# Kernel optimization log

Hardware: AMD Instinct MI355X
Metric: run time of the kernel (lower is better)

## Reference

```python
import jax, jax.numpy as jnp
import numpy as np

GN_GROUPS = 32
GN_EPS = 1e-5


def conv3x3(x, w, b=None):
    # x: [B,C,H,W], w: [O,I,3,3]
    y = jax.lax.conv_general_dilated(x, w, (1, 1), 'SAME',
                                     dimension_numbers=('NCHW', 'OIHW', 'NCHW'))
    if b is not None:
        y = y + b[None, :, None, None]
    return y


def group_norm(x, gamma, beta):
    B, C, H, W = x.shape
    xg = x.reshape(B, GN_GROUPS, C // GN_GROUPS, H, W)
    mu = xg.mean(axis=(2, 3, 4), keepdims=True)
    var = ((xg - mu) ** 2).mean(axis=(2, 3, 4), keepdims=True)
    xn = ((xg - mu) * jax.lax.rsqrt(var + GN_EPS)).reshape(B, C, H, W)
    return xn * gamma[None, :, None, None] + beta[None, :, None, None]


def tower(x, ws, gammas, betas):
    # ws: [n_conv, C, C, 3, 3]; conv(bias=False) -> GroupNorm -> ReLU, n_conv times
    for i in range(ws.shape[0]):
        x = jax.nn.relu(group_norm(conv3x3(x, ws[i]), gammas[i], betas[i]))
    return x


def setup_inputs() -> dict:
    key = jax.random.key(0)
    ks = jax.random.split(key, 20)
    C, n_conv, n_fg = 256, 4, 20  # n_class - 1 = 20
    prior = 0.01
    B = 2
    sizes = [(100, 100), (50, 50), (25, 25), (13, 13), (7, 7)]
    inp = {}
    for i, (h, w) in enumerate(sizes):
        inp[f'feat{i}'] = jax.random.normal(ks[i], (B, C, h, w), dtype=jnp.float32)
    std = 0.01  # init_conv_std
    inp['cls_tw_w'] = std * jax.random.normal(ks[5], (n_conv, C, C, 3, 3), dtype=jnp.float32)
    inp['cls_tw_g'] = jnp.ones((n_conv, C), dtype=jnp.float32)
    inp['cls_tw_b'] = jnp.zeros((n_conv, C), dtype=jnp.float32)
    inp['box_tw_w'] = std * jax.random.normal(ks[6], (n_conv, C, C, 3, 3), dtype=jnp.float32)
    inp['box_tw_g'] = jnp.ones((n_conv, C), dtype=jnp.float32)
    inp['box_tw_b'] = jnp.zeros((n_conv, C), dtype=jnp.float32)
    inp['cls_pred_w'] = std * jax.random.normal(ks[7], (n_fg, C, 3, 3), dtype=jnp.float32)
    prior_bias = -np.log((1.0 - prior) / prior)
    inp['cls_pred_b'] = jnp.full((n_fg,), prior_bias, dtype=jnp.float32)
    inp['box_pred_w'] = std * jax.random.normal(ks[8], (4, C, 3, 3), dtype=jnp.float32)
    inp['box_pred_b'] = jnp.zeros((4,), dtype=jnp.float32)
    inp['ctr_pred_w'] = std * jax.random.normal(ks[9], (1, C, 3, 3), dtype=jnp.float32)
    inp['ctr_pred_b'] = jnp.zeros((1,), dtype=jnp.float32)
    inp['scales'] = jnp.ones((5,), dtype=jnp.float32)
    return inp


def reference(feat0, feat1, feat2, feat3, feat4,
              cls_tw_w, cls_tw_g, cls_tw_b,
              box_tw_w, box_tw_g, box_tw_b,
              cls_pred_w, cls_pred_b,
              box_pred_w, box_pred_b,
              ctr_pred_w, ctr_pred_b,
              scales):
    feats = [feat0, feat1, feat2, feat3, feat4]
    logits, bboxes, centers = [], [], []
    for i, feat in enumerate(feats):
        c = tower(feat, cls_tw_w, cls_tw_g, cls_tw_b)
        logits.append(conv3x3(c, cls_pred_w, cls_pred_b))
        centers.append(conv3x3(c, ctr_pred_w, ctr_pred_b))
        b = tower(feat, box_tw_w, box_tw_g, box_tw_b)
        bboxes.append(jnp.exp(conv3x3(b, box_pred_w, box_pred_b) * scales[i]))
    return tuple(logits + bboxes + centers)
```

## Files before the change

kernel.cpp:

```cpp
#include <hip/hip_runtime.h>
#include <hip/hip_bf16.h>
#include <cstdint>

typedef unsigned short u16;
typedef __attribute__((ext_vector_type(8))) short short8;
typedef __attribute__((ext_vector_type(4))) float floatx4;
typedef __attribute__((ext_vector_type(4))) int intx4;

#define PA_TOTAL 13696
#define CCH 256
#define KTOT 2304

struct Tables {
  int H[5], W[5], P[5], base[5], tile0[5];
  int lb[5], bb[5], cb[5];
};
struct FeatPtrs { const float* f[5]; };
struct ConvArgs {
  const u16* X[2];
  const u16* Wt[2];
  const u16* zbuf;
  u16* outB[2];
  float* stats;
  float* dout;
  const float* biasCls; const float* biasCtr; const float* biasBox; const float* scales;
};

__device__ __forceinline__ u16 f2bf(float f) {
  union { float f; unsigned u; } v; v.f = f;
  unsigned r = v.u + 0x7fffu + ((v.u >> 16) & 1u);
  return (u16)(r >> 16);
}
__device__ __forceinline__ float bf2f(u16 h) {
  union { unsigned u; float f; } v; v.u = ((unsigned)h) << 16;
  return v.f;
}

__global__ void reorder_rows(const float* __restrict__ src, u16* __restrict__ out) {
  __shared__ float row[KTOT];
  const int r = blockIdx.x;
  const float* s = src + (size_t)r * KTOT;
  u16* o = out + (size_t)r * KTOT;
#pragma unroll
  for (int j = 0; j < 9; ++j) row[threadIdx.x + j * 256] = s[threadIdx.x + j * 256];
  __syncthreads();
#pragma unroll
  for (int j = 0; j < 9; ++j) {
    int k = threadIdx.x + j * 256;
    o[k] = f2bf(row[(k & 255) * 9 + (k >> 8)]);
  }
}

__global__ void reorder_pred_cls(const float* __restrict__ cls_w, const float* __restrict__ ctr_w,
                                 u16* __restrict__ out) {
  __shared__ float row[KTOT];
  const int r = blockIdx.x;
  const float* s = (r < 20) ? (cls_w + (size_t)r * KTOT) : ctr_w;
  u16* o = out + (size_t)r * KTOT;
#pragma unroll
  for (int j = 0; j < 9; ++j) row[threadIdx.x + j * 256] = s[threadIdx.x + j * 256];
  __syncthreads();
#pragma unroll
  for (int j = 0; j < 9; ++j) {
    int k = threadIdx.x + j * 256;
    o[k] = f2bf(row[(k & 255) * 9 + (k >> 8)]);
  }
}

__global__ void convert_inputs(FeatPtrs fp, u16* __restrict__ out, Tables tb) {
  __shared__ float tile[32][33];
  const int pt = blockIdx.x, c32 = blockIdx.y, b = blockIdx.z;
  const int p0 = pt * 32;
  int lvl = 0;
#pragma unroll
  for (int i = 1; i < 5; ++i) if (p0 >= tb.base[i]) lvl = i;
  const int P = tb.P[lvl];
  const int pl0 = p0 - tb.base[lvl];
  const int r = threadIdx.x >> 5, col = threadIdx.x & 31;
  const float* src = fp.f[lvl] + ((size_t)b * CCH + c32 * 32) * P;
#pragma unroll
  for (int i = 0; i < 4; ++i) {
    int crow = r + i * 8;
    int pl = pl0 + col;
    tile[crow][col] = (pl < P) ? src[(size_t)crow * P + pl] : 0.f;
  }
  __syncthreads();
#pragma unroll
  for (int i = 0; i < 4; ++i) {
    int px = r + i * 8;
    out[((size_t)b * PA_TOTAL + p0 + px) * CCH + c32 * 32 + col] = f2bf(tile[col][px]);
  }
}

template <int MODE>
__global__ __launch_bounds__(256) void conv_mfma(ConvArgs a, Tables tb) {
  constexpr int NI = (MODE == 0) ? 4 : 1;
  const int L = blockIdx.x + (MODE == 0 ? 107 : 108) * (blockIdx.y + 2 * blockIdx.z);
  const int xcd = L & 7, slot = L >> 3;
  int tower, mt, b, t;
  if (MODE == 0) {
    tower = xcd >> 2; mt = (xcd >> 1) & 1; b = xcd & 1; t = slot;
  } else {
    tower = xcd >> 2; mt = 0; b = (xcd >> 1) & 1; t = slot * 2 + (xcd & 1);
    if (t >= 107) return;
  }
  int lvl = 0;
#pragma unroll
  for (int i = 1; i < 5; ++i) if (t >= tb.tile0[i]) lvl = i;
  const int H = tb.H[lvl], W = tb.W[lvl], P = tb.P[lvl], base = tb.base[lvl];
  const int n0 = (t - tb.tile0[lvl]) * 128;

  const int tid = threadIdx.x;
  const int lane = tid & 63, wv = tid >> 6;
  const int wm = wv >> 1, wn = wv & 1;

  __shared__ u16 ldsX[128 * 64];
  __shared__ u16 ldsW[(MODE == 0 ? 128 : 32) * 64];

  const u16* X = a.X[tower];
  const u16* Wt = a.Wt[tower];

  const int qsw = (((lane & 7) ^ (lane >> 3))) * 8;
  int prow[4];
  unsigned mask9[4];
  int xdst[4];
#pragma unroll
  for (int t4 = 0; t4 < 4; ++t4) {
    int row = (t4 * 4 + wv) * 8 + (lane >> 3);
    prow[t4] = n0 + row;
    int rr = prow[t4] / W, cc = prow[t4] - rr * W;
    unsigned m = 0;
#pragma unroll
    for (int tap = 0; tap < 9; ++tap) {
      const int dh = tap / 3 - 1, dw = tap % 3 - 1;
      bool v = ((unsigned)(rr + dh) < (unsigned)H) & ((unsigned)(cc + dw) < (unsigned)W);
      m |= ((unsigned)v) << tap;
    }
    mask9[t4] = m;
    xdst[t4] = (t4 * 4 + wv) * 1024 + lane * 16;
  }
  const u16* wsrc[NI];
  int wdst[NI];
#pragma unroll
  for (int e = 0; e < NI; ++e) {
    int wrow = (MODE == 0) ? ((e * 4 + wv) * 8 + (lane >> 3)) : (wv * 8 + (lane >> 3));
    wsrc[e] = Wt + (size_t)(mt * 128 + wrow) * KTOT + qsw;
    wdst[e] = (MODE == 0) ? xdst[e] : (wv * 1024 + lane * 16);
  }
  const u16* Xbp = X + ((size_t)b * PA_TOTAL + base) * CCH;

  const int arow = lane & 15, rsw = lane & 7, kq0 = lane >> 4;
  int aoff[2][NI], boff[2][4];
#pragma unroll
  for (int h = 0; h < 2; ++h) {
    int csw = (((h * 4 + kq0) ^ rsw)) * 8;
#pragma unroll
    for (int i = 0; i < NI; ++i) {
      int rowb = (MODE == 0) ? (wm * 64 + i * 16) : (wm * 16);
      aoff[h][i] = (rowb + arow) * 64 + csw;
    }
#pragma unroll
    for (int i = 0; i < 4; ++i) boff[h][i] = (wn * 64 + i * 16 + arow) * 64 + csw;
  }

  floatx4 acc[NI][4];
#pragma unroll
  for (int i = 0; i < NI; ++i)
#pragma unroll
    for (int j = 0; j < 4; ++j) acc[i][j] = (floatx4)0.f;

  const intx4 zreg = {0, 0, 0, 0};
  intx4 xr[4], wr[NI];
  {
    const int dpos0 = -W - 1;
#pragma unroll
    for (int t4 = 0; t4 < 4; ++t4)
      xr[t4] = (mask9[t4] & 1)
          ? *(const intx4*)(Xbp + (size_t)(prow[t4] + dpos0) * CCH + qsw) : zreg;
#pragma unroll
    for (int e = 0; e < NI; ++e) wr[e] = *(const intx4*)(wsrc[e]);
  }

#pragma unroll 1
  for (int icb = 0; icb < 4; ++icb) {
#pragma unroll
    for (int tap = 0; tap < 9; ++tap) {
      __syncthreads();
#pragma unroll
      for (int t4 = 0; t4 < 4; ++t4) *(intx4*)((char*)ldsX + xdst[t4]) = xr[t4];
#pragma unroll
      for (int e = 0; e < NI; ++e) *(intx4*)((char*)ldsW + wdst[e]) = wr[e];
      if (!(icb == 3 && tap == 8)) {
        const int ntap = (tap == 8) ? 0 : tap + 1;
        const int nicb = (tap == 8) ? icb + 1 : icb;
        const int ndh = ntap / 3;
        const int ndpos = (ndh - 1) * W + (ntap - 3 * ndh - 1);
        const int nko = ntap * 256 + nicb * 64;
#pragma unroll
        for (int t4 = 0; t4 < 4; ++t4)
          xr[t4] = ((mask9[t4] >> ntap) & 1)
              ? *(const intx4*)(Xbp + (size_t)(prow[t4] + ndpos) * CCH + qsw + nicb * 64) : zreg;
#pragma unroll
        for (int e = 0; e < NI; ++e) wr[e] = *(const intx4*)(wsrc[e] + nko);
      }
      asm volatile("s_waitcnt lgkmcnt(0)\n\ts_barrier" ::: "memory");
#pragma unroll
      for (int h = 0; h < 2; ++h) {
        short8 af[NI], bv[4];
#pragma unroll
        for (int i = 0; i < NI; ++i) af[i] = *(const short8*)(ldsW + aoff[h][i]);
#pragma unroll
        for (int j = 0; j < 4; ++j) bv[j] = *(const short8*)(ldsX + boff[h][j]);
#pragma unroll
        for (int i = 0; i < NI; ++i)
#pragma unroll
          for (int j = 0; j < 4; ++j)
            acc[i][j] = __builtin_amdgcn_mfma_f32_16x16x32_bf16(af[i], bv[j], acc[i][j], 0, 0, 0);
      }
    }
  }

  const int quad = lane >> 4, col = lane & 15;
  if (MODE == 0) {
    u16* convB = a.outB[tower];
    float s[4] = {0.f, 0.f, 0.f, 0.f}, ss[4] = {0.f, 0.f, 0.f, 0.f};
#pragma unroll
    for (int j = 0; j < 4; ++j) {
      int pl = n0 + wn * 64 + j * 16 + col;
      bool valid = pl < P;
      u16* dst = convB + ((size_t)b * PA_TOTAL + base + pl) * CCH + mt * 128 + wm * 64 + quad * 4;
#pragma unroll
      for (int i = 0; i < 4; ++i) {
        ushort4 hv;
#pragma unroll
        for (int r = 0; r < 4; ++r) {
          u16 hh = f2bf(acc[i][j][r]);
          ((u16*)&hv)[r] = hh;
          float vr = bf2f(hh);
          if (valid) { s[i] += vr; ss[i] += vr * vr; }
        }
        if (valid) *(ushort4*)(dst + i * 16) = hv;
      }
    }
#pragma unroll
    for (int i = 0; i < 4; ++i) {
#pragma unroll
      for (int off = 16; off >= 1; off >>= 1) {
        s[i] += __shfl_down(s[i], off, 64);
        ss[i] += __shfl_down(ss[i], off, 64);
      }
    }
    if ((lane & 31) == 0) {
      int half = lane >> 5;
#pragma unroll
      for (int i = 0; i < 4; ++i) {
        float* st = a.stats + tower * 640 +
                    ((size_t)((b * 5 + lvl) * 32 + mt * 16 + wm * 8 + i * 2 + half)) * 2;
        atomicAdd(st, s[i]);
        atomicAdd(st + 1, ss[i]);
      }
    }
  } else {
    float* dout = a.dout;
    if (tower == 0) {
#pragma unroll
      for (int j = 0; j < 4; ++j) {
        int pl = n0 + wn * 64 + j * 16 + col;
        if (pl >= P) continue;
        int ocb = wm * 16 + quad * 4;
#pragma unroll
        for (int r = 0; r < 4; ++r) {
          int oc = ocb + r;
          float v = acc[0][j][r];
          if (oc < 20)       dout[tb.lb[lvl] + ((size_t)b * 20 + oc) * P + pl] = v + a.biasCls[oc];
          else if (oc == 20) dout[tb.cb[lvl] + (size_t)b * P + pl] = v + a.biasCtr[0];
        }
      }
    } else {
      float sc = a.scales[lvl];
#pragma unroll
      for (int j = 0; j < 4; ++j) {
        int pl = n0 + wn * 64 + j * 16 + col;
        if (pl >= P) continue;
        int ocb = wm * 16 + quad * 4;
#pragma unroll
        for (int r = 0; r < 4; ++r) {
          int oc = ocb + r;
          if (oc < 4)
            dout[tb.bb[lvl] + ((size_t)b * 4 + oc) * P + pl] = expf((acc[0][j][r] + a.biasBox[oc]) * sc);
        }
      }
    }
  }
}

__global__ void gn_norm(const u16* __restrict__ c0, const u16* __restrict__ c1,
                        const float* __restrict__ stats,
                        const float* __restrict__ g0, const float* __restrict__ b0,
                        const float* __restrict__ g1, const float* __restrict__ b1,
                        u16* __restrict__ a0, u16* __restrict__ a1, Tables tb) {
  const int tower = blockIdx.y;
  const u16* convB = tower ? c1 : c0;
  const float* gamma = tower ? g1 : g0;
  const float* beta = tower ? b1 : b0;
  u16* act = tower ? a1 : a0;
  int idx = blockIdx.x * 256 + threadIdx.x;
  int c8 = idx & 31;
  int rest = idx >> 5;
  int p = rest % PA_TOTAL;
  int b = rest / PA_TOTAL;
  int lvl = 0;
#pragma unroll
  for (int i = 1; i < 5; ++i) if (p >= tb.base[i]) lvl = i;
  if (p - tb.base[lvl] >= tb.P[lvl]) return;
  const float* st = stats + tower * 640 + ((size_t)((b * 5 + lvl) * 32 + c8)) * 2;
  float cnt = 8.f * (float)tb.P[lvl];
  float mean = st[0] / cnt;
  float var = st[1] / cnt - mean * mean;
  float inv = rsqrtf(var + 1e-5f);
  const short8 x = *(const short8*)(convB + ((size_t)b * PA_TOTAL + p) * CCH + c8 * 8);
  short8 o;
#pragma unroll
  for (int j = 0; j < 8; ++j) {
    float v = bf2f((u16)x[j]);
    float y = (v - mean) * inv * gamma[c8 * 8 + j] + beta[c8 * 8 + j];
    y = fmaxf(y, 0.f);
    o[j] = (short)f2bf(y);
  }
  *(short8*)(act + ((size_t)b * PA_TOTAL + p) * CCH + c8 * 8) = o;
}

extern "C" void kernel_launch(void* const* d_in, const int* in_sizes, int n_in,
                              void* d_out, int out_size, void* d_ws, size_t ws_size,
                              hipStream_t stream) {
  const float* feat[5];
  for (int i = 0; i < 5; ++i) feat[i] = (const float*)d_in[i];
  const float* cls_tw_w  = (const float*)d_in[5];
  const float* cls_tw_g  = (const float*)d_in[6];
  const float* cls_tw_b  = (const float*)d_in[7];
  const float* box_tw_w  = (const float*)d_in[8];
  const float* box_tw_g  = (const float*)d_in[9];
  const float* box_tw_b  = (const float*)d_in[10];
  const float* cls_pred_w = (const float*)d_in[11];
  const float* cls_pred_b = (const float*)d_in[12];
  const float* box_pred_w = (const float*)d_in[13];
  const float* box_pred_b = (const float*)d_in[14];
  const float* ctr_pred_w = (const float*)d_in[15];
  const float* ctr_pred_b = (const float*)d_in[16];
  const float* scales     = (const float*)d_in[17];
  float* out = (float*)d_out;

  char* ws = (char*)d_ws;
  u16*   zbuf   = (u16*)(ws);
  float* stats  = (float*)(ws + 512);
  u16*   WrCls  = (u16*)(ws + 8192);
  u16*   WrBox  = (u16*)(ws + 8192 + 4718592);
  u16*   WrPCls = (u16*)(ws + 8192 + 2 * 4718592);
  u16*   WrPBox = (u16*)(ws + 8192 + 2 * 4718592 + 589824);
  u16*   bufIn   = (u16*)(ws + 10625024);
  u16*   bufAct0 = (u16*)(ws + 10625024 + 1 * (size_t)14024704);
  u16*   bufAct1 = (u16*)(ws + 10625024 + 2 * (size_t)14024704);
  u16*   bufCv0  = (u16*)(ws + 10625024 + 3 * (size_t)14024704);
  u16*   bufCv1  = (u16*)(ws + 10625024 + 4 * (size_t)14024704);

  Tables tb = { {100,50,25,13,7}, {100,50,25,13,7}, {10000,2500,625,169,49},
                {0,10112,12672,13312,13568}, {0,79,99,104,106},
                {0,400000,500000,525000,531760},
                {533720,613720,633720,638720,640072},
                {640464,660464,665464,666714,667052} };

  hipMemsetAsync(zbuf, 0, 512, stream);
  hipMemsetAsync(WrPCls, 0, 589824, stream);
  hipMemsetAsync(WrPBox, 0, 589824, stream);

  reorder_rows<<<1024, 256, 0, stream>>>(cls_tw_w, WrCls);
  reorder_rows<<<1024, 256, 0, stream>>>(box_tw_w, WrBox);
  reorder_pred_cls<<<21, 256, 0, stream>>>(cls_pred_w, ctr_pred_w, WrPCls);
  reorder_rows<<<4, 256, 0, stream>>>(box_pred_w, WrPBox);

  FeatPtrs fp = {{feat[0], feat[1], feat[2], feat[3], feat[4]}};
  convert_inputs<<<dim3(PA_TOTAL / 32, 8, 2), 256, 0, stream>>>(fp, bufIn, tb);

  ConvArgs a;
  a.zbuf = zbuf; a.stats = stats; a.dout = out;
  a.biasCls = cls_pred_b; a.biasCtr = ctr_pred_b; a.biasBox = box_pred_b; a.scales = scales;
  a.outB[0] = bufCv0; a.outB[1] = bufCv1;

  for (int s = 0; s < 4; ++s) {
    a.X[0] = (s == 0) ? bufIn : bufAct0;
    a.X[1] = (s == 0) ? bufIn : bufAct1;
    a.Wt[0] = WrCls + (size_t)s * 256 * KTOT;
    a.Wt[1] = WrBox + (size_t)s * 256 * KTOT;
    hipMemsetAsync(stats, 0, 5120, stream);
    conv_mfma<0><<<dim3(107, 2, 4), 256, 0, stream>>>(a, tb);
    gn_norm<<<dim3(3424, 2), 256, 0, stream>>>(bufCv0, bufCv1, stats,
                                               cls_tw_g + s * 256, cls_tw_b + s * 256,
                                               box_tw_g + s * 256, box_tw_b + s * 256,
                                               bufAct0, bufAct1, tb);
  }
  a.X[0] = bufAct0; a.X[1] = bufAct1;
  a.Wt[0] = WrPCls; a.Wt[1] = WrPBox;
  conv_mfma<1><<<dim3(108, 2, 2), 256, 0, stream>>>(a, tb);
}
```

Measured before the change: 648.6 us.

## Load conv MFMA operands directly from global memory, dropping LDS staging

The implicit-GEMM conv kernel no longer stages X and W tiles through shared memory. Each wave now loads its MFMA fragments straight from global or cache, and out-of-bounds taps point at a zeroed padding row past each level. The gn_norm kernel is changed to write zeros into those padding rows so they can act as the zero source. Launch bounds request 3 blocks per CU and s_setprio is raised around the MFMA burst, aiming to remove LDS traffic and sync overhead at the cost of redundant global loads across waves and no software prefetch.

```diff
diff --git a/kernel.cpp b/kernel.cpp
--- a/kernel.cpp
+++ b/kernel.cpp
@@ -93,7 +93,7 @@
 }
 
 template <int MODE>
-__global__ __launch_bounds__(256) void conv_mfma(ConvArgs a, Tables tb) {
+__global__ __launch_bounds__(256, 3) void conv_mfma(ConvArgs a, Tables tb) {
   constexpr int NI = (MODE == 0) ? 4 : 1;
   const int L = blockIdx.x + (MODE == 0 ? 107 : 108) * (blockIdx.y + 2 * blockIdx.z);
   const int xcd = L & 7, slot = L >> 3;
@@ -114,21 +114,19 @@
   const int lane = tid & 63, wv = tid >> 6;
   const int wm = wv >> 1, wn = wv & 1;
 
-  __shared__ u16 ldsX[128 * 64];
-  __shared__ u16 ldsW[(MODE == 0 ? 128 : 32) * 64];
-
   const u16* X = a.X[tower];
   const u16* Wt = a.Wt[tower];
-
-  const int qsw = (((lane & 7) ^ (lane >> 3))) * 8;
-  int prow[4];
-  unsigned mask9[4];
-  int xdst[4];
-#pragma unroll
-  for (int t4 = 0; t4 < 4; ++t4) {
-    int row = (t4 * 4 + wv) * 8 + (lane >> 3);
-    prow[t4] = n0 + row;
-    int rr = prow[t4] / W, cc = prow[t4] - rr * W;
+  const char* Xbp = (const char*)(X + ((size_t)b * PA_TOTAL + base) * CCH);
+  const char* Wbp = (const char*)(Wt + (size_t)(MODE == 0 ? mt * 128 : 0) * KTOT);
+
+  const int fr = lane & 15;
+  const int klane2 = (lane >> 4) * 16;
+
+  unsigned voffX[4], mask9[4];
+#pragma unroll
+  for (int j = 0; j < 4; ++j) {
+    int rowj = n0 + wn * 64 + j * 16 + fr;
+    int rr = rowj / W, cc = rowj - rr * W;
     unsigned m = 0;
 #pragma unroll
     for (int tap = 0; tap < 9; ++tap) {
@@ -136,31 +134,16 @@
       bool v = ((unsigned)(rr + dh) < (unsigned)H) & ((unsigned)(cc + dw) < (unsigned)W);
       m |= ((unsigned)v) << tap;
     }
-    mask9[t4] = m;
-    xdst[t4] = (t4 * 4 + wv) * 1024 + lane * 16;
-  }
-  const u16* wsrc[NI];
-  int wdst[NI];
+    mask9[j] = m;
+    voffX[j] = (unsigned)(rowj * (CCH * 2)) + klane2;
+  }
+  const unsigned zb = (unsigned)(P * (CCH * 2)) + klane2;
+
+  unsigned voffW[NI];
 #pragma unroll
   for (int e = 0; e < NI; ++e) {
-    int wrow = (MODE == 0) ? ((e * 4 + wv) * 8 + (lane >> 3)) : (wv * 8 + (lane >> 3));
-    wsrc[e] = Wt + (size_t)(mt * 128 + wrow) * KTOT + qsw;
-    wdst[e] = (MODE == 0) ? xdst[e] : (wv * 1024 + lane * 16);
-  }
-  const u16* Xbp = X + ((size_t)b * PA_TOTAL + base) * CCH;
-
-  const int arow = lane & 15, rsw = lane & 7, kq0 = lane >> 4;
-  int aoff[2][NI], boff[2][4];
-#pragma unroll
-  for (int h = 0; h < 2; ++h) {
-    int csw = (((h * 4 + kq0) ^ rsw)) * 8;
-#pragma unroll
-    for (int i = 0; i < NI; ++i) {
-      int rowb = (MODE == 0) ? (wm * 64 + i * 16) : (wm * 16);
-      aoff[h][i] = (rowb + arow) * 64 + csw;
-    }
-#pragma unroll
-    for (int i = 0; i < 4; ++i) boff[h][i] = (wn * 64 + i * 16 + arow) * 64 + csw;
+    int wrow = (MODE == 0) ? (wm * 64 + e * 16 + fr) : (wm * 16 + fr);
+    voffW[e] = (unsigned)(wrow * (KTOT * 2)) + klane2;
   }
 
   floatx4 acc[NI][4];
@@ -168,55 +151,38 @@
   for (int i = 0; i < NI; ++i)
 #pragma unroll
     for (int j = 0; j < 4; ++j) acc[i][j] = (floatx4)0.f;
-
-  const intx4 zreg = {0, 0, 0, 0};
-  intx4 xr[4], wr[NI];
-  {
-    const int dpos0 = -W - 1;
-#pragma unroll
-    for (int t4 = 0; t4 < 4; ++t4)
-      xr[t4] = (mask9[t4] & 1)
-          ? *(const intx4*)(Xbp + (size_t)(prow[t4] + dpos0) * CCH + qsw) : zreg;
-#pragma unroll
-    for (int e = 0; e < NI; ++e) wr[e] = *(const intx4*)(wsrc[e]);
-  }
 
 #pragma unroll 1
   for (int icb = 0; icb < 4; ++icb) {
 #pragma unroll
     for (int tap = 0; tap < 9; ++tap) {
-      __syncthreads();
-#pragma unroll
-      for (int t4 = 0; t4 < 4; ++t4) *(intx4*)((char*)ldsX + xdst[t4]) = xr[t4];
-#pragma unroll
-      for (int e = 0; e < NI; ++e) *(intx4*)((char*)ldsW + wdst[e]) = wr[e];
-      if (!(icb == 3 && tap == 8)) {
-        const int ntap = (tap == 8) ? 0 : tap + 1;
-        const int nicb = (tap == 8) ? icb + 1 : icb;
-        const int ndh = ntap / 3;
-        const int ndpos = (ndh - 1) * W + (ntap - 3 * ndh - 1);
-        const int nko = ntap * 256 + nicb * 64;
-#pragma unroll
-        for (int t4 = 0; t4 < 4; ++t4)
-          xr[t4] = ((mask9[t4] >> ntap) & 1)
-              ? *(const intx4*)(Xbp + (size_t)(prow[t4] + ndpos) * CCH + qsw + nicb * 64) : zreg;
-#pragma unroll
-        for (int e = 0; e < NI; ++e) wr[e] = *(const intx4*)(wsrc[e] + nko);
-      }
-      asm volatile("s_waitcnt lgkmcnt(0)\n\ts_barrier" ::: "memory");
-#pragma unroll
-      for (int h = 0; h < 2; ++h) {
-        short8 af[NI], bv[4];
-#pragma unroll
-        for (int i = 0; i < NI; ++i) af[i] = *(const short8*)(ldsW + aoff[h][i]);
-#pragma unroll
-        for (int j = 0; j < 4; ++j) bv[j] = *(const short8*)(ldsX + boff[h][j]);
+      __builtin_amdgcn_s_barrier();
+      const int dh = tap / 3 - 1, dw = tap % 3 - 1;
+      const int soffX = (dh * W + dw) * (CCH * 2) + icb * 128;
+      const int koW = tap * 512 + icb * 128;
+      const char* ax = Xbp + soffX;
+      const char* aw = Wbp + koW;
+      short8 xf[2][4], wf[2][NI];
+#pragma unroll
+      for (int j = 0; j < 4; ++j) {
+        const unsigned vo = ((mask9[j] >> tap) & 1u) ? voffX[j] : (zb - (unsigned)soffX);
+        xf[0][j] = *(const short8*)(ax + vo);
+        xf[1][j] = *(const short8*)(ax + vo + 64);
+      }
+#pragma unroll
+      for (int e = 0; e < NI; ++e) {
+        wf[0][e] = *(const short8*)(aw + voffW[e]);
+        wf[1][e] = *(const short8*)(aw + voffW[e] + 64);
+      }
+      __builtin_amdgcn_s_setprio(1);
+#pragma unroll
+      for (int h = 0; h < 2; ++h)
 #pragma unroll
         for (int i = 0; i < NI; ++i)
 #pragma unroll
           for (int j = 0; j < 4; ++j)
-            acc[i][j] = __builtin_amdgcn_mfma_f32_16x16x32_bf16(af[i], bv[j], acc[i][j], 0, 0, 0);
-      }
+            acc[i][j] = __builtin_amdgcn_mfma_f32_16x16x32_bf16(wf[h][i], xf[h][j], acc[i][j], 0, 0, 0);
+      __builtin_amdgcn_s_setprio(0);
     }
   }
 
@@ -312,7 +278,11 @@
   int lvl = 0;
 #pragma unroll
   for (int i = 1; i < 5; ++i) if (p >= tb.base[i]) lvl = i;
-  if (p - tb.base[lvl] >= tb.P[lvl]) return;
+  if (p - tb.base[lvl] >= tb.P[lvl]) {
+    short8 z = (short8)(short)0;
+    *(short8*)(act + ((size_t)b * PA_TOTAL + p) * CCH + c8 * 8) = z;
+    return;
+  }
   const float* st = stats + tower * 640 + ((size_t)((b * 5 + lvl) * 32 + c8)) * 2;
   float cnt = 8.f * (float)tb.P[lvl];
   float mean = st[0] / cnt;
```

New measurement: 1.360 ms. +109.6%, slower.

## Fuse GroupNorm+ReLU into next conv's input load, remove gn_norm pass

Applied to the files above, without the earlier changes.

Removes the standalone gn_norm kernel. Normalization and ReLU are now applied in registers as each conv loads its raw bf16 input, with per-group coefficients computed from the previous layer's stats. Conv outputs ping-pong between two buffer pairs and two stats buffers, and padding taps are masked to zero after normalization. This avoids a full read and write of the activations per layer and a kernel launch. The cost is extra VALU work per tap in the conv inner loop, and launch_bounds now requests 4 blocks per CU, which may limit registers.

```diff
diff --git a/kernel.cpp b/kernel.cpp
--- a/kernel.cpp
+++ b/kernel.cpp
@@ -19,9 +19,11 @@
 struct ConvArgs {
   const u16* X[2];
   const u16* Wt[2];
-  const u16* zbuf;
   u16* outB[2];
   float* stats;
+  const float* statsIn;
+  const float* gG[2];
+  const float* gB[2];
   float* dout;
   const float* biasCls; const float* biasCtr; const float* biasBox; const float* scales;
 };
@@ -34,6 +36,32 @@
 __device__ __forceinline__ float bf2f(u16 h) {
   union { unsigned u; float f; } v; v.u = ((unsigned)h) << 16;
   return v.f;
+}
+
+__device__ __forceinline__ intx4 gn_relu(intx4 r, const float* A, const float* C) {
+  union { intx4 i; short8 s; } u; u.i = r;
+  short8 o;
+#pragma unroll
+  for (int j = 0; j < 8; ++j) {
+    float v = bf2f((u16)u.s[j]);
+    float y = fmaxf(fmaf(v, A[j], C[j]), 0.f);
+    o[j] = (short)f2bf(y);
+  }
+  union { short8 s; intx4 i; } w; w.s = o;
+  return w.i;
+}
+
+__device__ __forceinline__ void gn_coeff(const float* stT, const float* G0, const float* B0,
+                                         int icb, int qsw, float invcnt,
+                                         float* A, float* C) {
+  const float* st = stT + (size_t)(icb * 8 + (qsw >> 3)) * 2;
+  float mean = st[0] * invcnt;
+  float var  = fmaxf(st[1] * invcnt - mean * mean, 0.f);
+  float inv  = rsqrtf(var + 1e-5f);
+  const float* G = G0 + icb * 64 + qsw;
+  const float* B = B0 + icb * 64 + qsw;
+#pragma unroll
+  for (int j = 0; j < 8; ++j) { float g = G[j] * inv; A[j] = g; C[j] = B[j] - mean * g; }
 }
 
 __global__ void reorder_rows(const float* __restrict__ src, u16* __restrict__ out) {
@@ -92,8 +120,8 @@
   }
 }
 
-template <int MODE>
-__global__ __launch_bounds__(256) void conv_mfma(ConvArgs a, Tables tb) {
+template <int MODE, int FUSE>
+__global__ __launch_bounds__(256, 4) void conv_mfma(ConvArgs a, Tables tb) {
   constexpr int NI = (MODE == 0) ? 4 : 1;
   const int L = blockIdx.x + (MODE == 0 ? 107 : 108) * (blockIdx.y + 2 * blockIdx.z);
   const int xcd = L & 7, slot = L >> 3;
@@ -169,6 +197,12 @@
 #pragma unroll
     for (int j = 0; j < 4; ++j) acc[i][j] = (floatx4)0.f;
 
+  float A8[8], C8[8];
+  const float invcnt = FUSE ? (1.f / (8.f * (float)P)) : 0.f;
+  const float* stT = FUSE ? (a.statsIn + tower * 640 + (size_t)((b * 5 + lvl) * 32) * 2) : nullptr;
+  const float* gGt = FUSE ? a.gG[tower] : nullptr;
+  const float* gBt = FUSE ? a.gB[tower] : nullptr;
+
   const intx4 zreg = {0, 0, 0, 0};
   intx4 xr[4], wr[NI];
   {
@@ -179,6 +213,14 @@
           ? *(const intx4*)(Xbp + (size_t)(prow[t4] + dpos0) * CCH + qsw) : zreg;
 #pragma unroll
     for (int e = 0; e < NI; ++e) wr[e] = *(const intx4*)(wsrc[e]);
+    if (FUSE) {
+      gn_coeff(stT, gGt, gBt, 0, qsw, invcnt, A8, C8);
+#pragma unroll
+      for (int t4 = 0; t4 < 4; ++t4) {
+        intx4 tr = gn_relu(xr[t4], A8, C8);
+        xr[t4] = (mask9[t4] & 1u) ? tr : zreg;
+      }
+    }
   }
 
 #pragma unroll 1
@@ -217,6 +259,18 @@
           for (int j = 0; j < 4; ++j)
             acc[i][j] = __builtin_amdgcn_mfma_f32_16x16x32_bf16(af[i], bv[j], acc[i][j], 0, 0, 0);
       }
+      if (FUSE) {
+        if (!(icb == 3 && tap == 8)) {
+          const int ntap2 = (tap == 8) ? 0 : tap + 1;
+          if (tap == 8)
+            gn_coeff(stT, gGt, gBt, icb + 1, qsw, invcnt, A8, C8);
+#pragma unroll
+          for (int t4 = 0; t4 < 4; ++t4) {
+            intx4 tr = gn_relu(xr[t4], A8, C8);
+            xr[t4] = ((mask9[t4] >> ntap2) & 1u) ? tr : zreg;
+          }
+        }
+      }
     }
   }
 
@@ -292,42 +346,6 @@
       }
     }
   }
-}
-
-__global__ void gn_norm(const u16* __restrict__ c0, const u16* __restrict__ c1,
-                        const float* __restrict__ stats,
-                        const float* __restrict__ g0, const float* __restrict__ b0,
-                        const float* __restrict__ g1, const float* __restrict__ b1,
-                        u16* __restrict__ a0, u16* __restrict__ a1, Tables tb) {
-  const int tower = blockIdx.y;
-  const u16* convB = tower ? c1 : c0;
-  const float* gamma = tower ? g1 : g0;
-  const float* beta = tower ? b1 : b0;
-  u16* act = tower ? a1 : a0;
-  int idx = blockIdx.x * 256 + threadIdx.x;
-  int c8 = idx & 31;
-  int rest = idx >> 5;
-  int p = rest % PA_TOTAL;
-  int b = rest / PA_TOTAL;
-  int lvl = 0;
-#pragma unroll
-  for (int i = 1; i < 5; ++i) if (p >= tb.base[i]) lvl = i;
-  if (p - tb.base[lvl] >= tb.P[lvl]) return;
-  const float* st = stats + tower * 640 + ((size_t)((b * 5 + lvl) * 32 + c8)) * 2;
-  float cnt = 8.f * (float)tb.P[lvl];
-  float mean = st[0] / cnt;
-  float var = st[1] / cnt - mean * mean;
-  float inv = rsqrtf(var + 1e-5f);
-  const short8 x = *(const short8*)(convB + ((size_t)b * PA_TOTAL + p) * CCH + c8 * 8);
-  short8 o;
-#pragma unroll
-  for (int j = 0; j < 8; ++j) {
-    float v = bf2f((u16)x[j]);
-    float y = (v - mean) * inv * gamma[c8 * 8 + j] + beta[c8 * 8 + j];
-    y = fmaxf(y, 0.f);
-    o[j] = (short)f2bf(y);
-  }
-  *(short8*)(act + ((size_t)b * PA_TOTAL + p) * CCH + c8 * 8) = o;
 }
 
 extern "C" void kernel_launch(void* const* d_in, const int* in_sizes, int n_in,
@@ -351,17 +369,17 @@
   float* out = (float*)d_out;
 
   char* ws = (char*)d_ws;
-  u16*   zbuf   = (u16*)(ws);
-  float* stats  = (float*)(ws + 512);
+  float* statsA = (float*)(ws + 512);
   u16*   WrCls  = (u16*)(ws + 8192);
   u16*   WrBox  = (u16*)(ws + 8192 + 4718592);
-  u16*   WrPCls = (u16*)(ws + 8192 + 2 * 4718592);
-  u16*   WrPBox = (u16*)(ws + 8192 + 2 * 4718592 + 589824);
-  u16*   bufIn   = (u16*)(ws + 10625024);
-  u16*   bufAct0 = (u16*)(ws + 10625024 + 1 * (size_t)14024704);
-  u16*   bufAct1 = (u16*)(ws + 10625024 + 2 * (size_t)14024704);
-  u16*   bufCv0  = (u16*)(ws + 10625024 + 3 * (size_t)14024704);
-  u16*   bufCv1  = (u16*)(ws + 10625024 + 4 * (size_t)14024704);
+  u16*   WrPCls = (u16*)(ws + 9445376);
+  u16*   WrPBox = (u16*)(ws + 9445376 + 147456);
+  float* statsB = (float*)(ws + 9445376 + 2 * 147456);
+  u16*   bufIn  = (u16*)(ws + 10625024);
+  u16*   bufB0  = (u16*)(ws + 10625024 + 1 * (size_t)14024704);
+  u16*   bufB1  = (u16*)(ws + 10625024 + 2 * (size_t)14024704);
+  u16*   bufA0  = (u16*)(ws + 10625024 + 3 * (size_t)14024704);
+  u16*   bufA1  = (u16*)(ws + 10625024 + 4 * (size_t)14024704);
 
   Tables tb = { {100,50,25,13,7}, {100,50,25,13,7}, {10000,2500,625,169,49},
                 {0,10112,12672,13312,13568}, {0,79,99,104,106},
@@ -369,9 +387,8 @@
                 {533720,613720,633720,638720,640072},
                 {640464,660464,665464,666714,667052} };
 
-  hipMemsetAsync(zbuf, 0, 512, stream);
-  hipMemsetAsync(WrPCls, 0, 589824, stream);
-  hipMemsetAsync(WrPBox, 0, 589824, stream);
+  hipMemsetAsync(WrPCls, 0, 147456, stream);
+  hipMemsetAsync(WrPBox, 0, 147456, stream);
 
   reorder_rows<<<1024, 256, 0, stream>>>(cls_tw_w, WrCls);
   reorder_rows<<<1024, 256, 0, stream>>>(box_tw_w, WrBox);
@@ -382,23 +399,29 @@
   convert_inputs<<<dim3(PA_TOTAL / 32, 8, 2), 256, 0, stream>>>(fp, bufIn, tb);
 
   ConvArgs a;
-  a.zbuf = zbuf; a.stats = stats; a.dout = out;
+  a.dout = out;
   a.biasCls = cls_pred_b; a.biasCtr = ctr_pred_b; a.biasBox = box_pred_b; a.scales = scales;
-  a.outB[0] = bufCv0; a.outB[1] = bufCv1;
 
   for (int s = 0; s < 4; ++s) {
-    a.X[0] = (s == 0) ? bufIn : bufAct0;
-    a.X[1] = (s == 0) ? bufIn : bufAct1;
+    a.X[0] = (s == 0) ? bufIn : ((s & 1) ? bufA0 : bufB0);
+    a.X[1] = (s == 0) ? bufIn : ((s & 1) ? bufA1 : bufB1);
+    a.outB[0] = (s & 1) ? bufB0 : bufA0;
+    a.outB[1] = (s & 1) ? bufB1 : bufA1;
     a.Wt[0] = WrCls + (size_t)s * 256 * KTOT;
     a.Wt[1] = WrBox + (size_t)s * 256 * KTOT;
-    hipMemsetAsync(stats, 0, 5120, stream);
-    conv_mfma<0><<<dim3(107, 2, 4), 256, 0, stream>>>(a, tb);
-    gn_norm<<<dim3(3424, 2), 256, 0, stream>>>(bufCv0, bufCv1, stats,
-                                               cls_tw_g + s * 256, cls_tw_b + s * 256,
-                                               box_tw_g + s * 256, box_tw_b + s * 256,
-                                               bufAct0, bufAct1, tb);
-  }
-  a.X[0] = bufAct0; a.X[1] = bufAct1;
+    a.stats   = (s & 1) ? statsB : statsA;
+    a.statsIn = (s & 1) ? statsA : statsB;
+    int sp = (s > 0) ? (s - 1) : 0;
+    a.gG[0] = cls_tw_g + sp * 256; a.gB[0] = cls_tw_b + sp * 256;
+    a.gG[1] = box_tw_g + sp * 256; a.gB[1] = box_tw_b + sp * 256;
+    hipMemsetAsync(a.stats, 0, 5120, stream);
+    if (s == 0) conv_mfma<0, 0><<<dim3(107, 2, 4), 256, 0, stream>>>(a, tb);
+    else        conv_mfma<0, 1><<<dim3(107, 2, 4), 256, 0, stream>>>(a, tb);
+  }
+  a.X[0] = bufB0; a.X[1] = bufB1;
   a.Wt[0] = WrPCls; a.Wt[1] = WrPBox;
-  conv_mfma<1><<<dim3(108, 2, 2), 256, 0, stream>>>(a, tb);
-}
+  a.statsIn = statsB;
+  a.gG[0] = cls_tw_g + 3 * 256; a.gB[0] = cls_tw_b + 3 * 256;
+  a.gG[1] = box_tw_g + 3 * 256; a.gB[1] = box_tw_b + 3 * 256;
+  conv_mfma<1, 1><<<dim3(108, 2, 2), 256, 0, stream>>>(a, tb);
+}
```

After: 2.389 ms. 3.68x slower.
